# Performance work log

Measured on AMD Instinct MI355X. Metric: run time of the kernel, lower is better.

Reference implementation:

```python
import jax, jax.numpy as jnp
import numpy as np
from jax import lax

BS, NV, CTX = 16, 7, 1536
PLEN, STRIDE = 16, 8
PN = (CTX - PLEN) // STRIDE + 1 + 1  # 192: end replication-pad adds one patch
D, H, DFF, L, TW = 512, 8, 2048, 3, 336
DK = D // H
SCALE = DK ** -0.5  # lsa=False -> fixed scale
NF = D * PN


def setup_inputs() -> dict:
    key = jax.random.key(0)
    ks = iter(jax.random.split(key, 40))

    def p(*shape, s=0.02):
        return jax.random.normal(next(ks), shape, jnp.float32) * s

    z = jax.random.normal(next(ks), (BS, NV, CTX), jnp.float32)
    # simpowerlaw decay mask: -|t|^scale, causal (-inf for k>q), one copy per layer
    t = np.arange(PN)
    times = t[:, None] - t[None, :]
    m = -np.abs(times).astype(np.float32) ** 0.25
    m[times < 0] = -np.inf
    decay_mask = jnp.asarray(np.broadcast_to(m, (L, PN, PN)).copy())
    return dict(
        z=z,
        W_P=p(PLEN, D), b_P=jnp.zeros((D,), jnp.float32),
        W_pos=p(PN, D),
        Wq=p(L, D, D), bq=jnp.zeros((L, D), jnp.float32),
        Wk=p(L, D, D), bk=jnp.zeros((L, D), jnp.float32),
        Wv=p(L, D, D), bv=jnp.zeros((L, D), jnp.float32),
        Wo=p(L, D, D), bo=jnp.zeros((L, D), jnp.float32),
        ln1_g=jnp.ones((L, D), jnp.float32), ln1_b=jnp.zeros((L, D), jnp.float32),
        W1=p(L, D, DFF), b1=jnp.zeros((L, DFF), jnp.float32),
        W2=p(L, DFF, D), b2=jnp.zeros((L, D), jnp.float32),
        ln2_g=jnp.ones((L, D), jnp.float32), ln2_b=jnp.zeros((L, D), jnp.float32),
        W_head=p(NF, TW, s=0.005), b_head=jnp.zeros((TW,), jnp.float32),
        decay_mask=decay_mask,
    )


def _ln(x, g, b):
    mu = x.mean(-1, keepdims=True)
    var = ((x - mu) ** 2).mean(-1, keepdims=True)
    return g * (x - mu) * lax.rsqrt(var + 1e-5) + b


def _forward(z, W_P, b_P, W_pos, Wq, bq, Wk, bk, Wv, bv, Wo, bo,
             ln1_g, ln1_b, W1, b1, W2, b2, ln2_g, ln2_b, W_head, b_head, decay_mask):
    bs, nv, _ = z.shape
    # replication pad end by STRIDE, then unfold into patches
    zp = jnp.concatenate([z, jnp.repeat(z[..., -1:], STRIDE, axis=-1)], axis=-1)
    idx = jnp.arange(PN)[:, None] * STRIDE + jnp.arange(PLEN)[None, :]
    patches = zp[..., idx]                      # [bs,nv,PN,PLEN]
    x = patches @ W_P + b_P                     # [bs,nv,PN,D]
    B = bs * nv
    src = x.reshape(B, PN, D) + W_pos           # channel-independent batch
    prev = jnp.zeros((B, H, PN, PN), src.dtype)  # residual attention carry

    def layer(carry, p):
        s, pr = carry
        wq, bq_, wk, bk_, wv, bv_, wo, bo_, g1, e1, w1, c1, w2, c2, g2, e2, dm = p
        q = (s @ wq + bq_).reshape(B, PN, H, DK).transpose(0, 2, 1, 3)
        k = (s @ wk + bk_).reshape(B, PN, H, DK).transpose(0, 2, 1, 3)
        v = (s @ wv + bv_).reshape(B, PN, H, DK).transpose(0, 2, 1, 3)
        scores = jnp.einsum('bhqd,bhkd->bhqk', q, k) * SCALE + pr + dm
        attn = jax.nn.softmax(scores, axis=-1)
        o = jnp.einsum('bhqk,bhkd->bhqd', attn, v).transpose(0, 2, 1, 3).reshape(B, PN, D)
        o = o @ wo + bo_
        s = _ln(s + o, g1, e1)                  # post-norm
        ff = jax.nn.gelu(s @ w1 + c1, approximate=False) @ w2 + c2
        s = _ln(s + ff, g2, e2)
        return (s, scores), None

    (src, _), _ = lax.scan(
        layer, (src, prev),
        (Wq, bq, Wk, bk, Wv, bv, Wo, bo, ln1_g, ln1_b, W1, b1, W2, b2, ln2_g, ln2_b, decay_mask))

    # Flatten_Head (individual=False): [bs,nv,D,PN] -> [bs,nv,D*PN] -> target_window
    xo = src.reshape(bs, nv, PN, D).transpose(0, 1, 3, 2).reshape(bs, nv, NF)
    return xo @ W_head + b_head                 # [bs,nv,TW]


def reference(z, W_P, b_P, W_pos, Wq, bq, Wk, bk, Wv, bv, Wo, bo,
              ln1_g, ln1_b, W1, b1, W2, b2, ln2_g, ln2_b, W_head, b_head, decay_mask):
    return _forward(z, W_P, b_P, W_pos, Wq, bq, Wk, bk, Wv, bv, Wo, bo,
                    ln1_g, ln1_b, W1, b1, W2, b2, ln2_g, ln2_b, W_head, b_head, decay_mask)
```

## Files before the change

### kernel.cpp

```cpp
#include <hip/hip_runtime.h>
#include <math.h>

#define BSZ 16
#define NV 7
#define CTX 1536
#define PN 192
#define PLEN 16
#define STRIDE 8
#define D 512
#define H 8
#define DK 64
#define DFF 2048
#define LYR 3
#define TW 336
#define NB 112
#define RTOT (NB * PN)
#define NF (D * PN)
#define SCALE 0.125f

typedef __attribute__((ext_vector_type(8))) short s16x8;
typedef __attribute__((ext_vector_type(4))) short s16x4;
typedef __attribute__((ext_vector_type(4))) float f32x4;

__device__ __forceinline__ unsigned short f2b(float f) {
  unsigned u = __builtin_bit_cast(unsigned, f);
  u = u + 0x7fffu + ((u >> 16) & 1u);
  return (unsigned short)(u >> 16);
}
__device__ __forceinline__ float b2f(unsigned short h) {
  unsigned u = ((unsigned)h) << 16;
  return __builtin_bit_cast(float, u);
}
__device__ __forceinline__ unsigned cvtpk(float lo, float hi) {
  unsigned r;
  asm("v_cvt_pk_bf16_f32 %0, %1, %2" : "=v"(r) : "v"(lo), "v"(hi));
  return r;
}
__device__ __forceinline__ float fast_exp2(float x) {
  float r; asm("v_exp_f32 %0, %1" : "=v"(r) : "v"(x)); return r;
}
__device__ __forceinline__ float fast_rcp(float x) {
  float r; asm("v_rcp_f32 %0, %1" : "=v"(r) : "v"(x)); return r;
}

__device__ __forceinline__ void glld(const unsigned short* g, short* l) {
  __builtin_amdgcn_global_load_lds(
      (const __attribute__((address_space(1))) void*)g,
      (__attribute__((address_space(3))) void*)l, 16, 0, 0);
}

__device__ __forceinline__ float gelu(float x) {
  float x2 = x * x;
  float u2 = x * fmaf(0.1029492f, x2, 2.3021186f);
  u2 = fminf(fmaxf(u2, -60.f), 60.f);
  float w = fast_exp2(u2);
  return x * w * fast_rcp(w + 1.0f);
}

__global__ __launch_bounds__(256) void k_patch_embed(
    const float* __restrict__ z, const float* __restrict__ W_P,
    const float* __restrict__ b_P, const float* __restrict__ W_pos,
    unsigned short* __restrict__ s) {
  int r = blockIdx.x;
  int bi = r / PN, p = r % PN;
  __shared__ float pv[PLEN];
  if (threadIdx.x < PLEN) {
    int t = p * STRIDE + threadIdx.x;
    pv[threadIdx.x] = z[(size_t)bi * CTX + (t < CTX ? t : CTX - 1)];
  }
  __syncthreads();
  for (int c = threadIdx.x; c < D; c += 256) {
    float acc = b_P[c] + W_pos[p * D + c];
#pragma unroll
    for (int j = 0; j < PLEN; j++) acc += pv[j] * W_P[j * D + c];
    s[(size_t)r * D + c] = f2b(acc);
  }
}

__global__ __launch_bounds__(256) void k_wtz(
    const float* __restrict__ W, unsigned short* __restrict__ Wt, int K, int N,
    size_t sstride, size_t dstride) {
  __shared__ float tile[32][33];
  const float* Wz = W + (size_t)blockIdx.z * sstride;
  unsigned short* Wtz = Wt + (size_t)blockIdx.z * dstride;
  int n0 = blockIdx.x * 32, k0 = blockIdx.y * 32;
  int tx = threadIdx.x & 31, ty = threadIdx.x >> 5;
#pragma unroll
  for (int i = 0; i < 4; i++)
    tile[ty + 8 * i][tx] =
        (n0 + tx < N) ? Wz[(size_t)(k0 + ty + 8 * i) * N + n0 + tx] : 0.0f;
  __syncthreads();
#pragma unroll
  for (int i = 0; i < 4; i++)
    if (n0 + ty + 8 * i < N)
      Wtz[(size_t)(n0 + ty + 8 * i) * K + k0 + tx] = f2b(tile[tx][ty + 8 * i]);
}

enum { EPI_QKV = 0, EPI_RES = 1, EPI_GELU = 2 };

template <int EPI, int N, int K>
__global__ __launch_bounds__(256) void k_mgemm(
    const unsigned short* __restrict__ Ap, const unsigned short* __restrict__ Wt,
    const float* __restrict__ bias0, const float* __restrict__ bias1,
    const float* __restrict__ bias2, const unsigned short* __restrict__ res,
    unsigned short* __restrict__ out0, unsigned short* __restrict__ out1,
    unsigned short* __restrict__ out2) {
  __shared__ short smem[24576];
  constexpr int NSTEP = K / 32;
  const int nx = N >> 7;
  const int nwg = gridDim.x;
  const int orig = blockIdx.x;
  const int wgid = (orig & 7) * (nwg >> 3) + (orig >> 3);
  const int m0 = (wgid / nx) * 128, n0 = (wgid % nx) * 128;
  const int t = threadIdx.x;
  const int w = t >> 6, l = t & 63;
  const int wr = (w >> 1) * 64, wc = (w & 1) * 64;
  const int lr = l & 15, lq = l >> 4;
  const int rsw = ((lr >> 1) & 3) << 3;
  const int srow = w * 32 + (l >> 2);
  const int scol = 8 * ((l & 3) ^ ((l >> 3) & 3));
  const unsigned short* gA = Ap + (size_t)(m0 + srow) * K + scol;
  const unsigned short* gB = Wt + (size_t)(n0 + srow) * K + scol;
  const int sbo = (w * 32) * 32;
  f32x4 acc[4][4] = {};

  auto STAGE = [&](int b, int kt) {
    short* dA = &smem[b * 8192 + sbo];
    short* dB = &smem[b * 8192 + 4096 + sbo];
    const int k0 = kt * 32;
    glld(gA + k0, dA);
    glld(gA + k0 + (size_t)16 * K, dA + 512);
    glld(gB + k0, dB);
    glld(gB + k0 + (size_t)16 * K, dB + 512);
  };

  STAGE(0, 0);
  STAGE(1, 1);
  int bc = 0, bs = 2;
  for (int step = 0; step < NSTEP; step++) {
    if (step + 2 < NSTEP) STAGE(bs, step + 2);
    if (step + 2 < NSTEP)      asm volatile("s_waitcnt vmcnt(8)" ::: "memory");
    else if (step + 1 < NSTEP) asm volatile("s_waitcnt vmcnt(4)" ::: "memory");
    else                       asm volatile("s_waitcnt vmcnt(0)" ::: "memory");
    __builtin_amdgcn_s_barrier();
    const short* cA = &smem[bc * 8192];
    const short* cB = &smem[bc * 8192 + 4096];
    s16x8 af[4], bf[4];
#pragma unroll
    for (int i = 0; i < 4; i++)
      af[i] = *(const s16x8*)&cA[(wr + i * 16 + lr) * 32 + ((lq * 8) ^ rsw)];
#pragma unroll
    for (int i = 0; i < 4; i++)
      bf[i] = *(const s16x8*)&cB[(wc + i * 16 + lr) * 32 + ((lq * 8) ^ rsw)];
#pragma unroll
    for (int i = 0; i < 4; i++)
#pragma unroll
      for (int j2 = 0; j2 < 4; j2++)
        acc[i][j2] = __builtin_amdgcn_mfma_f32_16x16x32_bf16(bf[j2], af[i], acc[i][j2], 0, 0, 0);
    asm volatile("s_waitcnt lgkmcnt(0)" ::: "memory");
    __builtin_amdgcn_s_barrier();
    bc++; if (bc == 3) bc = 0;
    bs++; if (bs == 3) bs = 0;
  }

  short* ot = smem;
  {
#pragma unroll
    for (int i = 0; i < 4; i++) {
      const int ml = wr + i * 16 + lr;
#pragma unroll
      for (int j2 = 0; j2 < 4; j2++) {
        const int nl = wc + j2 * 16 + lq * 4;
        f32x4 a = acc[i][j2];
        float4 b4 = *(const float4*)&bias0[n0 + nl];
        float v0 = a[0] + b4.x, v1 = a[1] + b4.y;
        float v2 = a[2] + b4.z, v3 = a[3] + b4.w;
        if (EPI == EPI_GELU) {
          v0 = gelu(v0); v1 = gelu(v1); v2 = gelu(v2); v3 = gelu(v3);
        } else {
          s16x4 rr = *(const s16x4*)&res[(size_t)(m0 + ml) * N + n0 + nl];
          v0 += b2f((unsigned short)rr[0]); v1 += b2f((unsigned short)rr[1]);
          v2 += b2f((unsigned short)rr[2]); v3 += b2f((unsigned short)rr[3]);
        }
        unsigned lo = cvtpk(v0, v1), hi = cvtpk(v2, v3);
        unsigned* d = (unsigned*)&ot[ml * 128 + ((nl >> 3) ^ (ml & 15)) * 8 + (nl & 7)];
        d[0] = lo; d[1] = hi;
      }
    }
    __syncthreads();
    const int r0 = t >> 1, cb = (t & 1) * 8;
    const size_t orow = (size_t)(m0 + r0) * N + n0;
#pragma unroll
    for (int q = 0; q < 8; q++) {
      int c = cb + q;
      s16x8 vv = *(const s16x8*)&ot[r0 * 128 + ((c ^ (r0 & 15)) * 8)];
      *(s16x8*)&out0[orow + c * 8] = vv;
    }
  }
}

template <int EPI, int N, int K>
__global__ __launch_bounds__(512, 2) void k_mgemm2(
    const unsigned short* __restrict__ Ap, const unsigned short* __restrict__ Wt,
    const float* __restrict__ bias0, const float* __restrict__ bias1,
    const float* __restrict__ bias2,
    unsigned short* __restrict__ out0, unsigned short* __restrict__ out1,
    unsigned short* __restrict__ out2) {
  __shared__ short smem[65536];
  constexpr int NSTEP = K / 64;
  const int nx = N >> 8;
  const int nwg = gridDim.x;
  const int orig = blockIdx.x;
  const int wgid = (orig & 7) * (nwg >> 3) + (orig >> 3);
  const int m0 = (wgid / nx) * 256, n0 = (wgid % nx) * 256;
  const int t = threadIdx.x;
  const int w = t >> 6, l = t & 63;
  const int wm = w >> 2, wn = w & 3;
  const int lr = l & 15, lq = l >> 4;
  const int srow = (w & 3) * 64 + (l >> 3);
  const int scol = ((l & 7) ^ (l >> 3)) * 8;
  const unsigned short* gsrc =
      (w < 4) ? (Ap + (size_t)(m0 + srow) * K + scol)
              : (Wt + (size_t)(n0 + srow) * K + scol);
  short* sdst = &smem[(w >= 4 ? 16384 : 0) + (w & 3) * 4096];
  f32x4 acc[8][4] = {};

  auto STAGE = [&](int b, int kt) {
    short* d = sdst + b * 32768;
    const unsigned short* g = gsrc + kt * 64;
#pragma unroll
    for (int q = 0; q < 8; q++)
      glld(g + (size_t)q * 8 * K, d + q * 512);
  };

  STAGE(0, 0);
  for (int step = 0; step < NSTEP; step++) {
    const int b = step & 1;
    if (step + 1 < NSTEP) {
      STAGE(b ^ 1, step + 1);
      asm volatile("s_waitcnt vmcnt(8)" ::: "memory");
    } else {
      asm volatile("s_waitcnt vmcnt(0)" ::: "memory");
    }
    __builtin_amdgcn_s_barrier();
    const short* cA = &smem[b * 32768];
    const short* cB = &smem[b * 32768 + 16384];
#pragma unroll
    for (int kk = 0; kk < 2; kk++) {
      s16x8 af[8], bf[4];
#pragma unroll
      for (int i = 0; i < 8; i++)
        af[i] = *(const s16x8*)&cA[(wm * 128 + i * 16 + lr) * 64 +
                                   (((kk * 4 + lq) ^ (lr & 7)) * 8)];
#pragma unroll
      for (int j = 0; j < 4; j++)
        bf[j] = *(const s16x8*)&cB[(wn * 64 + j * 16 + lr) * 64 +
                                   (((kk * 4 + lq) ^ (lr & 7)) * 8)];
      __builtin_amdgcn_s_setprio(1);
#pragma unroll
      for (int i = 0; i < 8; i++)
#pragma unroll
        for (int j = 0; j < 4; j++)
          acc[i][j] = __builtin_amdgcn_mfma_f32_16x16x32_bf16(bf[j], af[i], acc[i][j], 0, 0, 0);
      __builtin_amdgcn_s_setprio(0);
    }
    asm volatile("s_waitcnt lgkmcnt(0)" ::: "memory");
    __builtin_amdgcn_s_barrier();
  }

  short* ot = smem;
  if (EPI == EPI_QKV) {
    const int which = n0 >> 9;
    const int ccb = n0 & 511;
    const float* bias = (which == 0) ? bias0 : (which == 1) ? bias1 : bias2;
    unsigned short* dst = (which == 0) ? out0 : (which == 1) ? out1 : out2;
    if (which < 2) {
#pragma unroll
      for (int i = 0; i < 8; i++) {
        const int ml = wm * 128 + i * 16 + lr;
#pragma unroll
        for (int j = 0; j < 4; j++) {
          const int nl = wn * 64 + j * 16 + lq * 4;
          f32x4 a = acc[i][j];
          float4 b4 = *(const float4*)&bias[ccb + nl];
          unsigned lo = cvtpk(a[0] + b4.x, a[1] + b4.y);
          unsigned hi = cvtpk(a[2] + b4.z, a[3] + b4.w);
          unsigned* d = (unsigned*)&ot[ml * 256 + ((nl >> 3) ^ (ml & 15)) * 8 + (nl & 7)];
          d[0] = lo; d[1] = hi;
        }
      }
      __syncthreads();
      const int r0 = t >> 1, cb = (t & 1) * 16;
      const int m = m0 + r0;
      const int bi2 = m / PN, p = m % PN;
#pragma unroll
      for (int q = 0; q < 16; q++) {
        int c = cb + q;
        int cc = ccb + c * 8;
        int hh = cc >> 6, dk8 = cc & 63;
        s16x8 vv = *(const s16x8*)&ot[r0 * 256 + ((c ^ (r0 & 15)) * 8)];
        *(s16x8*)&dst[(((size_t)bi2 * H + hh) * PN + p) * DK + dk8] = vv;
      }
    } else {
#pragma unroll
      for (int i = 0; i < 8; i++) {
        const int m = m0 + wm * 128 + i * 16 + lr;
        const int bi2 = m / PN, p = m % PN;
#pragma unroll
        for (int j = 0; j < 4; j++) {
          const int nl = wn * 64 + j * 16 + lq * 4;
          f32x4 a = acc[i][j];
#pragma unroll
          for (int r = 0; r < 4; r++) {
            int cc = ccb + nl + r;
            int hh = cc >> 6, dkk = cc & 63;
            dst[(((size_t)bi2 * H + hh) * DK + dkk) * PN + p] = f2b(a[r] + bias[cc]);
          }
        }
      }
    }
  } else {
#pragma unroll
    for (int i = 0; i < 8; i++) {
      const int ml = wm * 128 + i * 16 + lr;
#pragma unroll
      for (int j = 0; j < 4; j++) {
        const int nl = wn * 64 + j * 16 + lq * 4;
        f32x4 a = acc[i][j];
        float4 b4 = *(const float4*)&bias0[n0 + nl];
        float v0 = gelu(a[0] + b4.x), v1 = gelu(a[1] + b4.y);
        float v2 = gelu(a[2] + b4.z), v3 = gelu(a[3] + b4.w);
        unsigned lo = cvtpk(v0, v1), hi = cvtpk(v2, v3);
        unsigned* d = (unsigned*)&ot[ml * 256 + ((nl >> 3) ^ (ml & 15)) * 8 + (nl & 7)];
        d[0] = lo; d[1] = hi;
      }
    }
    __syncthreads();
    const int r0 = t >> 1, cb = (t & 1) * 16;
    const size_t orow = (size_t)(m0 + r0) * N + n0;
#pragma unroll
    for (int q = 0; q < 16; q++) {
      int c = cb + q;
      s16x8 vv = *(const s16x8*)&ot[r0 * 256 + ((c ^ (r0 & 15)) * 8)];
      *(s16x8*)&out0[orow + c * 8] = vv;
    }
  }
}

#define PSTR 196
template <int FIRST, int WRITEC>
__global__ __launch_bounds__(256) void k_attn(
    const unsigned short* __restrict__ qb, const unsigned short* __restrict__ kb,
    const unsigned short* __restrict__ vt, const float* __restrict__ dm,
    unsigned short* __restrict__ carry, unsigned short* __restrict__ ob) {
  __shared__ short Ps[96 * PSTR];
  __shared__ float redmax[2][96];
  __shared__ float redsum[2][96];
  int blk = blockIdx.x;
  int bh = blk >> 1, qh = blk & 1;
  int bi = bh >> 3, h = bh & 7;
  int t = threadIdx.x, w = t >> 6, l = t & 63;
  int wq = w >> 1, wk = w & 1;
  int lr = l & 15, lq = l >> 4, lk = lq * 8;
  const unsigned short* Q = qb + (size_t)bh * PN * DK + (size_t)qh * 96 * DK;
  const unsigned short* K = kb + (size_t)bh * PN * DK;
  f32x4 sv[3][6] = {};
#pragma unroll
  for (int ks = 0; ks < 2; ks++) {
    s16x8 af[3], bf[6];
#pragma unroll
    for (int i = 0; i < 3; i++)
      af[i] = *(const s16x8*)&Q[(size_t)(wq * 48 + i * 16 + lr) * DK + ks * 32 + lk];
#pragma unroll
    for (int j = 0; j < 6; j++)
      bf[j] = *(const s16x8*)&K[(size_t)(wk * 96 + j * 16 + lr) * DK + ks * 32 + lk];
#pragma unroll
    for (int i = 0; i < 3; i++)
#pragma unroll
      for (int j = 0; j < 6; j++)
        sv[i][j] = __builtin_amdgcn_mfma_f32_16x16x32_bf16(af[i], bf[j], sv[i][j], 0, 0, 0);
  }
  size_t cbase = (size_t)blk * 18432 + (size_t)(w * 18) * 256 + (size_t)l * 4;
#pragma unroll
  for (int i = 0; i < 3; i++) {
#pragma unroll
    for (int j = 0; j < 6; j++) {
      s16x4 cv;
      if (!FIRST) cv = *(const s16x4*)&carry[cbase + (i * 6 + j) * 256];
      s16x4 cw;
#pragma unroll
      for (int r = 0; r < 4; r++) {
        int row = qh * 96 + wq * 48 + i * 16 + lq * 4 + r;
        int col = wk * 96 + j * 16 + lr;
        float v = sv[i][j][r] * SCALE + dm[row * PN + col];
        if (!FIRST) v += b2f((unsigned short)cv[r]);
        if (WRITEC) cw[r] = (short)f2b(v);
        sv[i][j][r] = v;
      }
      if (WRITEC) *(s16x4*)&carry[cbase + (i * 6 + j) * 256] = cw;
    }
  }
#pragma unroll
  for (int i = 0; i < 3; i++) {
#pragma unroll
    for (int r = 0; r < 4; r++) {
      float m = sv[i][0][r];
#pragma unroll
      for (int j = 1; j < 6; j++) m = fmaxf(m, sv[i][j][r]);
#pragma unroll
      for (int off = 1; off < 16; off <<= 1) m = fmaxf(m, __shfl_xor(m, off));
      if (lr == 0) redmax[wk][wq * 48 + i * 16 + lq * 4 + r] = m;
    }
  }
  __syncthreads();
#pragma unroll
  for (int i = 0; i < 3; i++) {
#pragma unroll
    for (int r = 0; r < 4; r++) {
      int row = wq * 48 + i * 16 + lq * 4 + r;
      float fm = fmaxf(redmax[0][row], redmax[1][row]);
      float sum = 0.f;
#pragma unroll
      for (int j = 0; j < 6; j++) {
        float e = __expf(sv[i][j][r] - fm);
        sum += e;
        Ps[row * PSTR + wk * 96 + j * 16 + lr] = f2b(e);
      }
#pragma unroll
      for (int off = 1; off < 16; off <<= 1) sum += __shfl_xor(sum, off);
      if (lr == 0) redsum[wk][row] = sum;
    }
  }
  __syncthreads();
  const unsigned short* V = vt + (size_t)bh * DK * PN;
  f32x4 po[3][2] = {};
#pragma unroll
  for (int ks = 0; ks < 6; ks++) {
    s16x8 af[3], bf[2];
#pragma unroll
    for (int i = 0; i < 3; i++)
      af[i] = *(const s16x8*)&Ps[(wq * 48 + i * 16 + lr) * PSTR + ks * 32 + lk];
#pragma unroll
    for (int j = 0; j < 2; j++)
      bf[j] = *(const s16x8*)&V[(size_t)(wk * 32 + j * 16 + lr) * PN + ks * 32 + lk];
#pragma unroll
    for (int i = 0; i < 3; i++)
#pragma unroll
      for (int j = 0; j < 2; j++)
        po[i][j] = __builtin_amdgcn_mfma_f32_16x16x32_bf16(af[i], bf[j], po[i][j], 0, 0, 0);
  }
#pragma unroll
  for (int i = 0; i < 3; i++) {
#pragma unroll
    for (int r = 0; r < 4; r++) {
      int row = wq * 48 + i * 16 + lq * 4 + r;
      float inv = 1.0f / (redsum[0][row] + redsum[1][row]);
#pragma unroll
      for (int j = 0; j < 2; j++) {
        int dk = wk * 32 + j * 16 + lr;
        ob[((size_t)bi * PN + qh * 96 + row) * D + h * 64 + dk] = f2b(po[i][j][r] * inv);
      }
    }
  }
}

__global__ __launch_bounds__(256) void k_ln(
    const unsigned short* __restrict__ in, const float* __restrict__ g,
    const float* __restrict__ b, unsigned short* __restrict__ out) {
  int r = blockIdx.x * 4 + (threadIdx.x >> 6);
  int l = threadIdx.x & 63;
  const unsigned short* x = in + (size_t)r * D + l * 8;
  s16x8 xv = *(const s16x8*)x;
  float v[8], sm = 0.f, sq = 0.f;
#pragma unroll
  for (int j = 0; j < 8; j++) {
    v[j] = b2f((unsigned short)xv[j]);
    sm += v[j];
    sq += v[j] * v[j];
  }
#pragma unroll
  for (int off = 32; off > 0; off >>= 1) {
    sm += __shfl_xor(sm, off);
    sq += __shfl_xor(sq, off);
  }
  float mu = sm * (1.0f / D);
  float rs = rsqrtf(sq * (1.0f / D) - mu * mu + 1e-5f);
  float4 g0 = *(const float4*)&g[l * 8], g1 = *(const float4*)&g[l * 8 + 4];
  float4 b0 = *(const float4*)&b[l * 8], b1 = *(const float4*)&b[l * 8 + 4];
  float gg[8] = {g0.x, g0.y, g0.z, g0.w, g1.x, g1.y, g1.z, g1.w};
  float bb[8] = {b0.x, b0.y, b0.z, b0.w, b1.x, b1.y, b1.z, b1.w};
  s16x8 ov;
#pragma unroll
  for (int j = 0; j < 8; j++) ov[j] = (short)f2b(gg[j] * (v[j] - mu) * rs + bb[j]);
  *(s16x8*)(out + (size_t)r * D + l * 8) = ov;
}

__global__ __launch_bounds__(256) void k_transpose_b(
    const unsigned short* __restrict__ sb, unsigned short* __restrict__ xo) {
  __shared__ unsigned short tile[32][33];
  int d0 = blockIdx.x * 32, p0 = blockIdx.y * 32, bv = blockIdx.z;
  int tx = threadIdx.x & 31, ty = threadIdx.x >> 5;
#pragma unroll
  for (int i = 0; i < 4; i++)
    tile[ty + 8 * i][tx] = sb[((size_t)bv * PN + p0 + ty + 8 * i) * D + d0 + tx];
  __syncthreads();
#pragma unroll
  for (int i = 0; i < 4; i++)
    xo[(size_t)bv * NF + (size_t)(d0 + ty + 8 * i) * PN + p0 + tx] = tile[tx][ty + 8 * i];
}

__global__ __launch_bounds__(448) void k_head_mgemm(
    const unsigned short* __restrict__ A, const unsigned short* __restrict__ B,
    float* __restrict__ pp) {
  __shared__ short As[112 * 40];
  __shared__ short Bs[336 * 40];
  int kc = blockIdx.x;
  int t = threadIdx.x, w = t >> 6, l = t & 63;
  int lr = l & 15, lk = (l >> 4) * 8;
  int ar = t >> 2, ac = (t & 3) * 8;
  f32x4 acc[7][3] = {};
  for (int ks = 0; ks < 24; ks++) {
    int k0 = kc * 768 + ks * 32;
    s16x8 av = *(const s16x8*)&A[(size_t)ar * NF + k0 + ac];
    s16x8 bv0, bv1, bv2;
    {
      int i0 = t, i1 = t + 448, i2 = t + 896;
      bv0 = *(const s16x8*)&B[(size_t)(i0 >> 2) * NF + k0 + (i0 & 3) * 8];
      bv1 = *(const s16x8*)&B[(size_t)(i1 >> 2) * NF + k0 + (i1 & 3) * 8];
      bv2 = *(const s16x8*)&B[(size_t)(i2 >> 2) * NF + k0 + (i2 & 3) * 8];
    }
    __syncthreads();
    *(s16x8*)&As[ar * 40 + ac] = av;
    *(s16x8*)&Bs[(t >> 2) * 40 + (t & 3) * 8] = bv0;
    *(s16x8*)&Bs[((t + 448) >> 2) * 40 + (t & 3) * 8] = bv1;
    *(s16x8*)&Bs[((t + 896) >> 2) * 40 + (t & 3) * 8] = bv2;
    __syncthreads();
    s16x8 bf[3];
#pragma unroll
    for (int j = 0; j < 3; j++)
      bf[j] = *(const s16x8*)&Bs[((w * 3 + j) * 16 + lr) * 40 + lk];
#pragma unroll
    for (int mf = 0; mf < 7; mf++) {
      s16x8 af = *(const s16x8*)&As[(mf * 16 + lr) * 40 + lk];
#pragma unroll
      for (int j = 0; j < 3; j++)
        acc[mf][j] = __builtin_amdgcn_mfma_f32_16x16x32_bf16(af, bf[j], acc[mf][j], 0, 0, 0);
    }
  }
#pragma unroll
  for (int mf = 0; mf < 7; mf++) {
#pragma unroll
    for (int j = 0; j < 3; j++) {
#pragma unroll
      for (int r = 0; r < 4; r++) {
        int row = mf * 16 + (l >> 4) * 4 + r;
        int col = (w * 3 + j) * 16 + lr;
        pp[((size_t)kc * NB + row) * TW + col] = acc[mf][j][r];
      }
    }
  }
}

__global__ __launch_bounds__(256) void k_head_reduce(
    const float* __restrict__ pp, const float* __restrict__ bh,
    float* __restrict__ out) {
  int i = blockIdx.x * 256 + threadIdx.x;
  float s = bh[i % TW];
  for (int kc = 0; kc < 128; kc++) s += pp[(size_t)kc * (NB * TW) + i];
  out[i] = s;
}

extern "C" void kernel_launch(void* const* d_in, const int* in_sizes, int n_in,
                              void* d_out, int out_size, void* d_ws, size_t ws_size,
                              hipStream_t stream) {
  const float* z     = (const float*)d_in[0];
  const float* W_P   = (const float*)d_in[1];
  const float* b_P   = (const float*)d_in[2];
  const float* W_pos = (const float*)d_in[3];
  const float* Wq    = (const float*)d_in[4];
  const float* bq    = (const float*)d_in[5];
  const float* Wk    = (const float*)d_in[6];
  const float* bk    = (const float*)d_in[7];
  const float* Wv    = (const float*)d_in[8];
  const float* bv    = (const float*)d_in[9];
  const float* Wo    = (const float*)d_in[10];
  const float* bo    = (const float*)d_in[11];
  const float* ln1g  = (const float*)d_in[12];
  const float* ln1b  = (const float*)d_in[13];
  const float* W1    = (const float*)d_in[14];
  const float* b1    = (const float*)d_in[15];
  const float* W2    = (const float*)d_in[16];
  const float* b2    = (const float*)d_in[17];
  const float* ln2g  = (const float*)d_in[18];
  const float* ln2b  = (const float*)d_in[19];
  const float* Wh    = (const float*)d_in[20];
  const float* bh    = (const float*)d_in[21];
  const float* dmask = (const float*)d_in[22];
  float* out = (float*)d_out;

  char* ws = (char*)d_ws;
  unsigned short* s  = (unsigned short*)ws;
  unsigned short* sc = (unsigned short*)(ws + 22020096ull);
  unsigned short* qb = (unsigned short*)(ws + 88080384ull);
  unsigned short* kb = (unsigned short*)(ws + 110100480ull);
  unsigned short* vb = (unsigned short*)(ws + 132120576ull);
  unsigned short* ob = (unsigned short*)(ws + 154140672ull);
  unsigned short* tb = (unsigned short*)(ws + 176160768ull);
  unsigned short* hb = qb;
  unsigned short* t2 = tb;
  unsigned short* wt = (unsigned short*)(ws + 198180864ull);
  const size_t WLS = 3145728;
  unsigned short* xo  = (unsigned short*)(ws + 88080384ull);
  unsigned short* Wht = (unsigned short*)(ws + 110100480ull);
  float* pp = (float*)(ws + 22020096ull);

  k_patch_embed<<<RTOT, 256, 0, stream>>>(z, W_P, b_P, W_pos, s);

  k_wtz<<<dim3(16, 16, 3), 256, 0, stream>>>(Wq, wt + 0,       D, D,   262144, WLS);
  k_wtz<<<dim3(16, 16, 3), 256, 0, stream>>>(Wk, wt + 262144,  D, D,   262144, WLS);
  k_wtz<<<dim3(16, 16, 3), 256, 0, stream>>>(Wv, wt + 524288,  D, D,   262144, WLS);
  k_wtz<<<dim3(16, 16, 3), 256, 0, stream>>>(Wo, wt + 786432,  D, D,   262144, WLS);
  k_wtz<<<dim3(64, 16, 3), 256, 0, stream>>>(W1, wt + 1048576, D, DFF, 1048576, WLS);
  k_wtz<<<dim3(16, 64, 3), 256, 0, stream>>>(W2, wt + 2097152, DFF, D, 1048576, WLS);

  for (int l = 0; l < LYR; l++) {
    unsigned short* wtL = wt + (size_t)l * WLS;
    unsigned short* wqkv_t = wtL;
    unsigned short* wo_t   = wtL + 786432;
    unsigned short* w1_t   = wtL + 1048576;
    unsigned short* w2_t   = wtL + 2097152;

    k_mgemm2<EPI_QKV, 1536, 512><<<504, 512, 0, stream>>>(
        s, wqkv_t, bq + l * D, bk + l * D, bv + l * D, qb, kb, vb);
    const float* dm = dmask + (size_t)l * PN * PN;
    if (l == 0)
      k_attn<1, 1><<<NB * H * 2, 256, 0, stream>>>(qb, kb, vb, dm, sc, ob);
    else if (l == LYR - 1)
      k_attn<0, 0><<<NB * H * 2, 256, 0, stream>>>(qb, kb, vb, dm, sc, ob);
    else
      k_attn<0, 1><<<NB * H * 2, 256, 0, stream>>>(qb, kb, vb, dm, sc, ob);
    k_mgemm<EPI_RES, 512, 512><<<672, 256, 0, stream>>>(
        ob, wo_t, bo + l * D, nullptr, nullptr, s, tb, nullptr, nullptr);
    k_ln<<<RTOT / 4, 256, 0, stream>>>(tb, ln1g + l * D, ln1b + l * D, s);
    k_mgemm2<EPI_GELU, 2048, 512><<<672, 512, 0, stream>>>(
        s, w1_t, b1 + l * DFF, nullptr, nullptr, hb, nullptr, nullptr);
    k_mgemm<EPI_RES, 512, 2048><<<672, 256, 0, stream>>>(
        hb, w2_t, b2 + l * D, nullptr, nullptr, s, t2, nullptr, nullptr);
    k_ln<<<RTOT / 4, 256, 0, stream>>>(t2, ln2g + l * D, ln2b + l * D, s);
  }

  k_wtz<<<dim3(11, 3072, 1), 256, 0, stream>>>(Wh, Wht, NF, TW, 0, 0);
  k_transpose_b<<<dim3(16, 6, NB), 256, 0, stream>>>(s, xo);
  k_head_mgemm<<<128, 448, 0, stream>>>(xo, Wht, pp);
  k_head_reduce<<<147, 256, 0, stream>>>(pp, bh, out);
}
```

Measured before the change: 1.106 ms.

## Unify GEMMs into one 256x256 kernel with interleaved LDS-load/MFMA pipeline

Merges the 128x128 and 256x256 GEMM kernels into a single 256x256-tile, 512-thread kernel that handles QKV, residual and GELU epilogues. The main loop is split into four MFMA quadrants, and the next tile's A and B global-to-LDS loads are issued between them so memory traffic overlaps compute. Barriers and s_setprio bracket each quadrant. The output-projection and FFN2 GEMMs (N=512) now use 168 large tiles instead of 672 small ones, which cuts redundant operand loads but leaves fewer workgroups to fill the GPU.

Result: no change. 1.120 ms (+1.3%).

```diff
diff --git a/kernel.cpp b/kernel.cpp
--- a/kernel.cpp
+++ b/kernel.cpp
@@ -99,79 +99,189 @@
 enum { EPI_QKV = 0, EPI_RES = 1, EPI_GELU = 2 };
 
 template <int EPI, int N, int K>
-__global__ __launch_bounds__(256) void k_mgemm(
+__global__ __launch_bounds__(512, 2) void k_mgemm2(
     const unsigned short* __restrict__ Ap, const unsigned short* __restrict__ Wt,
     const float* __restrict__ bias0, const float* __restrict__ bias1,
     const float* __restrict__ bias2, const unsigned short* __restrict__ res,
     unsigned short* __restrict__ out0, unsigned short* __restrict__ out1,
     unsigned short* __restrict__ out2) {
-  __shared__ short smem[24576];
-  constexpr int NSTEP = K / 32;
-  const int nx = N >> 7;
+  __shared__ short smem[65536];
+  constexpr int NT = K / 64;
+  const int nx = N >> 8;
   const int nwg = gridDim.x;
   const int orig = blockIdx.x;
   const int wgid = (orig & 7) * (nwg >> 3) + (orig >> 3);
-  const int m0 = (wgid / nx) * 128, n0 = (wgid % nx) * 128;
+  const int m0 = (wgid / nx) * 256, n0 = (wgid % nx) * 256;
   const int t = threadIdx.x;
   const int w = t >> 6, l = t & 63;
-  const int wr = (w >> 1) * 64, wc = (w & 1) * 64;
+  const int wm = w >> 2, wn = w & 3;
   const int lr = l & 15, lq = l >> 4;
-  const int rsw = ((lr >> 1) & 3) << 3;
-  const int srow = w * 32 + (l >> 2);
-  const int scol = 8 * ((l & 3) ^ ((l >> 3) & 3));
-  const unsigned short* gA = Ap + (size_t)(m0 + srow) * K + scol;
-  const unsigned short* gB = Wt + (size_t)(n0 + srow) * K + scol;
-  const int sbo = (w * 32) * 32;
-  f32x4 acc[4][4] = {};
-
-  auto STAGE = [&](int b, int kt) {
-    short* dA = &smem[b * 8192 + sbo];
-    short* dB = &smem[b * 8192 + 4096 + sbo];
-    const int k0 = kt * 32;
-    glld(gA + k0, dA);
-    glld(gA + k0 + (size_t)16 * K, dA + 512);
-    glld(gB + k0, dB);
-    glld(gB + k0 + (size_t)16 * K, dB + 512);
+  const int sr8 = w * 8 + (l >> 3);
+  const int sc8 = ((l & 7) ^ ((l >> 3) & 7)) * 8;
+  const unsigned short* gAs = Ap + (size_t)(m0 + sr8) * K + sc8;
+  const unsigned short* gBs = Wt + (size_t)(n0 + sr8) * K + sc8;
+  f32x4 acc[8][4] = {};
+
+  auto STA = [&](int bb, int kt, int h) {
+    short* d = &smem[bb * 32768 + (h * 128 + w * 8) * 64];
+    const unsigned short* g = gAs + (size_t)(h * 128) * K + kt * 64;
+    glld(g, d);
+    glld(g + (size_t)64 * K, d + 4096);
   };
-
-  STAGE(0, 0);
-  STAGE(1, 1);
-  int bc = 0, bs = 2;
-  for (int step = 0; step < NSTEP; step++) {
-    if (step + 2 < NSTEP) STAGE(bs, step + 2);
-    if (step + 2 < NSTEP)      asm volatile("s_waitcnt vmcnt(8)" ::: "memory");
-    else if (step + 1 < NSTEP) asm volatile("s_waitcnt vmcnt(4)" ::: "memory");
-    else                       asm volatile("s_waitcnt vmcnt(0)" ::: "memory");
+  auto STB = [&](int bb, int kt, int h) {
+    short* d = &smem[bb * 32768 + 16384 + (h * 128 + w * 8) * 64];
+    const unsigned short* g = gBs + (size_t)(h * 128) * K + kt * 64;
+    glld(g, d);
+    glld(g + (size_t)64 * K, d + 4096);
+  };
+
+  STA(0, 0, 0); STA(0, 0, 1); STB(0, 0, 0); STB(0, 0, 1);
+  asm volatile("s_waitcnt vmcnt(0)" ::: "memory");
+  __builtin_amdgcn_s_barrier();
+
+  for (int kt = 0; kt < NT; kt++) {
+    const int bb = kt & 1;
+    const short* cA = &smem[bb * 32768];
+    const short* cB = &smem[bb * 32768 + 16384];
+    s16x8 af0[4][2], af1[4][2], bf0[2][2], bf1[2][2];
+#pragma unroll
+    for (int i = 0; i < 4; i++)
+#pragma unroll
+      for (int kk = 0; kk < 2; kk++)
+        af0[i][kk] = *(const s16x8*)&cA[(wm * 128 + i * 16 + lr) * 64 +
+                                        (((kk * 4 + lq) ^ (lr & 7)) * 8)];
+#pragma unroll
+    for (int j = 0; j < 2; j++)
+#pragma unroll
+      for (int kk = 0; kk < 2; kk++)
+        bf0[j][kk] = *(const s16x8*)&cB[(wn * 64 + j * 16 + lr) * 64 +
+                                        (((kk * 4 + lq) ^ (lr & 7)) * 8)];
+    if (kt + 1 < NT) { STA(bb ^ 1, kt + 1, 0); STA(bb ^ 1, kt + 1, 1); }
     __builtin_amdgcn_s_barrier();
-    const short* cA = &smem[bc * 8192];
-    const short* cB = &smem[bc * 8192 + 4096];
-    s16x8 af[4], bf[4];
+    asm volatile("s_waitcnt lgkmcnt(0)" ::: "memory");
+    __builtin_amdgcn_s_setprio(1);
+#pragma unroll
+    for (int kk = 0; kk < 2; kk++)
+#pragma unroll
+      for (int i = 0; i < 4; i++)
+#pragma unroll
+        for (int j = 0; j < 2; j++)
+          acc[i][j] = __builtin_amdgcn_mfma_f32_16x16x32_bf16(
+              bf0[j][kk], af0[i][kk], acc[i][j], 0, 0, 0);
+    __builtin_amdgcn_s_setprio(0);
+    __builtin_amdgcn_s_barrier();
+#pragma unroll
+    for (int j = 0; j < 2; j++)
+#pragma unroll
+      for (int kk = 0; kk < 2; kk++)
+        bf1[j][kk] = *(const s16x8*)&cB[(wn * 64 + (2 + j) * 16 + lr) * 64 +
+                                        (((kk * 4 + lq) ^ (lr & 7)) * 8)];
+    if (kt + 1 < NT) { STB(bb ^ 1, kt + 1, 0); STB(bb ^ 1, kt + 1, 1); }
+    __builtin_amdgcn_s_barrier();
+    asm volatile("s_waitcnt lgkmcnt(0)" ::: "memory");
+    __builtin_amdgcn_s_setprio(1);
+#pragma unroll
+    for (int kk = 0; kk < 2; kk++)
+#pragma unroll
+      for (int i = 0; i < 4; i++)
+#pragma unroll
+        for (int j = 0; j < 2; j++)
+          acc[i][2 + j] = __builtin_amdgcn_mfma_f32_16x16x32_bf16(
+              bf1[j][kk], af0[i][kk], acc[i][2 + j], 0, 0, 0);
+    __builtin_amdgcn_s_setprio(0);
+    __builtin_amdgcn_s_barrier();
 #pragma unroll
     for (int i = 0; i < 4; i++)
-      af[i] = *(const s16x8*)&cA[(wr + i * 16 + lr) * 32 + ((lq * 8) ^ rsw)];
-#pragma unroll
-    for (int i = 0; i < 4; i++)
-      bf[i] = *(const s16x8*)&cB[(wc + i * 16 + lr) * 32 + ((lq * 8) ^ rsw)];
-#pragma unroll
-    for (int i = 0; i < 4; i++)
-#pragma unroll
-      for (int j2 = 0; j2 < 4; j2++)
-        acc[i][j2] = __builtin_amdgcn_mfma_f32_16x16x32_bf16(bf[j2], af[i], acc[i][j2], 0, 0, 0);
+#pragma unroll
+      for (int kk = 0; kk < 2; kk++)
+        af1[i][kk] = *(const s16x8*)&cA[(wm * 128 + 64 + i * 16 + lr) * 64 +
+                                        (((kk * 4 + lq) ^ (lr & 7)) * 8)];
+    __builtin_amdgcn_s_barrier();
     asm volatile("s_waitcnt lgkmcnt(0)" ::: "memory");
+    __builtin_amdgcn_s_setprio(1);
+#pragma unroll
+    for (int kk = 0; kk < 2; kk++)
+#pragma unroll
+      for (int i = 0; i < 4; i++)
+#pragma unroll
+        for (int j = 0; j < 2; j++)
+          acc[4 + i][j] = __builtin_amdgcn_mfma_f32_16x16x32_bf16(
+              bf0[j][kk], af1[i][kk], acc[4 + i][j], 0, 0, 0);
+    __builtin_amdgcn_s_setprio(0);
     __builtin_amdgcn_s_barrier();
-    bc++; if (bc == 3) bc = 0;
-    bs++; if (bs == 3) bs = 0;
+    __builtin_amdgcn_s_setprio(1);
+#pragma unroll
+    for (int kk = 0; kk < 2; kk++)
+#pragma unroll
+      for (int i = 0; i < 4; i++)
+#pragma unroll
+        for (int j = 0; j < 2; j++)
+          acc[4 + i][2 + j] = __builtin_amdgcn_mfma_f32_16x16x32_bf16(
+              bf1[j][kk], af1[i][kk], acc[4 + i][2 + j], 0, 0, 0);
+    __builtin_amdgcn_s_setprio(0);
+    asm volatile("s_waitcnt vmcnt(0)" ::: "memory");
+    __builtin_amdgcn_s_barrier();
   }
 
   short* ot = smem;
-  {
-#pragma unroll
-    for (int i = 0; i < 4; i++) {
-      const int ml = wr + i * 16 + lr;
-#pragma unroll
-      for (int j2 = 0; j2 < 4; j2++) {
-        const int nl = wc + j2 * 16 + lq * 4;
-        f32x4 a = acc[i][j2];
+  if (EPI == EPI_QKV) {
+    const int which = n0 >> 9;
+    const int ccb = n0 & 511;
+    const float* bias = (which == 0) ? bias0 : (which == 1) ? bias1 : bias2;
+    unsigned short* dst = (which == 0) ? out0 : (which == 1) ? out1 : out2;
+    if (which < 2) {
+#pragma unroll
+      for (int i = 0; i < 8; i++) {
+        const int ml = wm * 128 + i * 16 + lr;
+#pragma unroll
+        for (int j = 0; j < 4; j++) {
+          const int nl = wn * 64 + j * 16 + lq * 4;
+          f32x4 a = acc[i][j];
+          float4 b4 = *(const float4*)&bias[ccb + nl];
+          unsigned lo = cvtpk(a[0] + b4.x, a[1] + b4.y);
+          unsigned hi = cvtpk(a[2] + b4.z, a[3] + b4.w);
+          unsigned* d = (unsigned*)&ot[ml * 256 + ((nl >> 3) ^ (ml & 15)) * 8 + (nl & 7)];
+          d[0] = lo; d[1] = hi;
+        }
+      }
+      __syncthreads();
+      const int r0 = t >> 1, cb = (t & 1) * 16;
+      const int m = m0 + r0;
+      const int bi2 = m / PN, p = m % PN;
+#pragma unroll
+      for (int q = 0; q < 16; q++) {
+        int c = cb + q;
+        int cc = ccb + c * 8;
+        int hh = cc >> 6, dk8 = cc & 63;
+        s16x8 vv = *(const s16x8*)&ot[r0 * 256 + ((c ^ (r0 & 15)) * 8)];
+        *(s16x8*)&dst[(((size_t)bi2 * H + hh) * PN + p) * DK + dk8] = vv;
+      }
+    } else {
+#pragma unroll
+      for (int i = 0; i < 8; i++) {
+        const int m = m0 + wm * 128 + i * 16 + lr;
+        const int bi2 = m / PN, p = m % PN;
+#pragma unroll
+        for (int j = 0; j < 4; j++) {
+          const int nl = wn * 64 + j * 16 + lq * 4;
+          f32x4 a = acc[i][j];
+#pragma unroll
+          for (int r = 0; r < 4; r++) {
+            int cc = ccb + nl + r;
+            int hh = cc >> 6, dkk = cc & 63;
+            dst[(((size_t)bi2 * H + hh) * DK + dkk) * PN + p] = f2b(a[r] + bias[cc]);
+          }
+        }
+      }
+    }
+  } else {
+#pragma unroll
+    for (int i = 0; i < 8; i++) {
+      const int ml = wm * 128 + i * 16 + lr;
+#pragma unroll
+      for (int j = 0; j < 4; j++) {
+        const int nl = wn * 64 + j * 16 + lq * 4;
+        f32x4 a = acc[i][j];
         float4 b4 = *(const float4*)&bias0[n0 + nl];
         float v0 = a[0] + b4.x, v1 = a[1] + b4.y;
         float v2 = a[2] + b4.z, v3 = a[3] + b4.w;
@@ -182,154 +292,6 @@
           v0 += b2f((unsigned short)rr[0]); v1 += b2f((unsigned short)rr[1]);
           v2 += b2f((unsigned short)rr[2]); v3 += b2f((unsigned short)rr[3]);
         }
-        unsigned lo = cvtpk(v0, v1), hi = cvtpk(v2, v3);
-        unsigned* d = (unsigned*)&ot[ml * 128 + ((nl >> 3) ^ (ml & 15)) * 8 + (nl & 7)];
-        d[0] = lo; d[1] = hi;
-      }
-    }
-    __syncthreads();
-    const int r0 = t >> 1, cb = (t & 1) * 8;
-    const size_t orow = (size_t)(m0 + r0) * N + n0;
-#pragma unroll
-    for (int q = 0; q < 8; q++) {
-      int c = cb + q;
-      s16x8 vv = *(const s16x8*)&ot[r0 * 128 + ((c ^ (r0 & 15)) * 8)];
-      *(s16x8*)&out0[orow + c * 8] = vv;
-    }
-  }
-}
-
-template <int EPI, int N, int K>
-__global__ __launch_bounds__(512, 2) void k_mgemm2(
-    const unsigned short* __restrict__ Ap, const unsigned short* __restrict__ Wt,
-    const float* __restrict__ bias0, const float* __restrict__ bias1,
-    const float* __restrict__ bias2,
-    unsigned short* __restrict__ out0, unsigned short* __restrict__ out1,
-    unsigned short* __restrict__ out2) {
-  __shared__ short smem[65536];
-  constexpr int NSTEP = K / 64;
-  const int nx = N >> 8;
-  const int nwg = gridDim.x;
-  const int orig = blockIdx.x;
-  const int wgid = (orig & 7) * (nwg >> 3) + (orig >> 3);
-  const int m0 = (wgid / nx) * 256, n0 = (wgid % nx) * 256;
-  const int t = threadIdx.x;
-  const int w = t >> 6, l = t & 63;
-  const int wm = w >> 2, wn = w & 3;
-  const int lr = l & 15, lq = l >> 4;
-  const int srow = (w & 3) * 64 + (l >> 3);
-  const int scol = ((l & 7) ^ (l >> 3)) * 8;
-  const unsigned short* gsrc =
-      (w < 4) ? (Ap + (size_t)(m0 + srow) * K + scol)
-              : (Wt + (size_t)(n0 + srow) * K + scol);
-  short* sdst = &smem[(w >= 4 ? 16384 : 0) + (w & 3) * 4096];
-  f32x4 acc[8][4] = {};
-
-  auto STAGE = [&](int b, int kt) {
-    short* d = sdst + b * 32768;
-    const unsigned short* g = gsrc + kt * 64;
-#pragma unroll
-    for (int q = 0; q < 8; q++)
-      glld(g + (size_t)q * 8 * K, d + q * 512);
-  };
-
-  STAGE(0, 0);
-  for (int step = 0; step < NSTEP; step++) {
-    const int b = step & 1;
-    if (step + 1 < NSTEP) {
-      STAGE(b ^ 1, step + 1);
-      asm volatile("s_waitcnt vmcnt(8)" ::: "memory");
-    } else {
-      asm volatile("s_waitcnt vmcnt(0)" ::: "memory");
-    }
-    __builtin_amdgcn_s_barrier();
-    const short* cA = &smem[b * 32768];
-    const short* cB = &smem[b * 32768 + 16384];
-#pragma unroll
-    for (int kk = 0; kk < 2; kk++) {
-      s16x8 af[8], bf[4];
-#pragma unroll
-      for (int i = 0; i < 8; i++)
-        af[i] = *(const s16x8*)&cA[(wm * 128 + i * 16 + lr) * 64 +
-                                   (((kk * 4 + lq) ^ (lr & 7)) * 8)];
-#pragma unroll
-      for (int j = 0; j < 4; j++)
-        bf[j] = *(const s16x8*)&cB[(wn * 64 + j * 16 + lr) * 64 +
-                                   (((kk * 4 + lq) ^ (lr & 7)) * 8)];
-      __builtin_amdgcn_s_setprio(1);
-#pragma unroll
-      for (int i = 0; i < 8; i++)
-#pragma unroll
-        for (int j = 0; j < 4; j++)
-          acc[i][j] = __builtin_amdgcn_mfma_f32_16x16x32_bf16(bf[j], af[i], acc[i][j], 0, 0, 0);
-      __builtin_amdgcn_s_setprio(0);
-    }
-    asm volatile("s_waitcnt lgkmcnt(0)" ::: "memory");
-    __builtin_amdgcn_s_barrier();
-  }
-
-  short* ot = smem;
-  if (EPI == EPI_QKV) {
-    const int which = n0 >> 9;
-    const int ccb = n0 & 511;
-    const float* bias = (which == 0) ? bias0 : (which == 1) ? bias1 : bias2;
-    unsigned short* dst = (which == 0) ? out0 : (which == 1) ? out1 : out2;
-    if (which < 2) {
-#pragma unroll
-      for (int i = 0; i < 8; i++) {
-        const int ml = wm * 128 + i * 16 + lr;
-#pragma unroll
-        for (int j = 0; j < 4; j++) {
-          const int nl = wn * 64 + j * 16 + lq * 4;
-          f32x4 a = acc[i][j];
-          float4 b4 = *(const float4*)&bias[ccb + nl];
-          unsigned lo = cvtpk(a[0] + b4.x, a[1] + b4.y);
-          unsigned hi = cvtpk(a[2] + b4.z, a[3] + b4.w);
-          unsigned* d = (unsigned*)&ot[ml * 256 + ((nl >> 3) ^ (ml & 15)) * 8 + (nl & 7)];
-          d[0] = lo; d[1] = hi;
-        }
-      }
-      __syncthreads();
-      const int r0 = t >> 1, cb = (t & 1) * 16;
-      const int m = m0 + r0;
-      const int bi2 = m / PN, p = m % PN;
-#pragma unroll
-      for (int q = 0; q < 16; q++) {
-        int c = cb + q;
-        int cc = ccb + c * 8;
-        int hh = cc >> 6, dk8 = cc & 63;
-        s16x8 vv = *(const s16x8*)&ot[r0 * 256 + ((c ^ (r0 & 15)) * 8)];
-        *(s16x8*)&dst[(((size_t)bi2 * H + hh) * PN + p) * DK + dk8] = vv;
-      }
-    } else {
-#pragma unroll
-      for (int i = 0; i < 8; i++) {
-        const int m = m0 + wm * 128 + i * 16 + lr;
-        const int bi2 = m / PN, p = m % PN;
-#pragma unroll
-        for (int j = 0; j < 4; j++) {
-          const int nl = wn * 64 + j * 16 + lq * 4;
-          f32x4 a = acc[i][j];
-#pragma unroll
-          for (int r = 0; r < 4; r++) {
-            int cc = ccb + nl + r;
-            int hh = cc >> 6, dkk = cc & 63;
-            dst[(((size_t)bi2 * H + hh) * DK + dkk) * PN + p] = f2b(a[r] + bias[cc]);
-          }
-        }
-      }
-    }
-  } else {
-#pragma unroll
-    for (int i = 0; i < 8; i++) {
-      const int ml = wm * 128 + i * 16 + lr;
-#pragma unroll
-      for (int j = 0; j < 4; j++) {
-        const int nl = wn * 64 + j * 16 + lq * 4;
-        f32x4 a = acc[i][j];
-        float4 b4 = *(const float4*)&bias0[n0 + nl];
-        float v0 = gelu(a[0] + b4.x), v1 = gelu(a[1] + b4.y);
-        float v2 = gelu(a[2] + b4.z), v3 = gelu(a[3] + b4.w);
         unsigned lo = cvtpk(v0, v1), hi = cvtpk(v2, v3);
         unsigned* d = (unsigned*)&ot[ml * 256 + ((nl >> 3) ^ (ml & 15)) * 8 + (nl & 7)];
         d[0] = lo; d[1] = hi;
@@ -631,7 +593,7 @@
     unsigned short* w2_t   = wtL + 2097152;
 
     k_mgemm2<EPI_QKV, 1536, 512><<<504, 512, 0, stream>>>(
-        s, wqkv_t, bq + l * D, bk + l * D, bv + l * D, qb, kb, vb);
+        s, wqkv_t, bq + l * D, bk + l * D, bv + l * D, nullptr, qb, kb, vb);
     const float* dm = dmask + (size_t)l * PN * PN;
     if (l == 0)
       k_attn<1, 1><<<NB * H * 2, 256, 0, stream>>>(qb, kb, vb, dm, sc, ob);
@@ -639,12 +601,12 @@
       k_attn<0, 0><<<NB * H * 2, 256, 0, stream>>>(qb, kb, vb, dm, sc, ob);
     else
       k_attn<0, 1><<<NB * H * 2, 256, 0, stream>>>(qb, kb, vb, dm, sc, ob);
-    k_mgemm<EPI_RES, 512, 512><<<672, 256, 0, stream>>>(
+    k_mgemm2<EPI_RES, 512, 512><<<168, 512, 0, stream>>>(
         ob, wo_t, bo + l * D, nullptr, nullptr, s, tb, nullptr, nullptr);
     k_ln<<<RTOT / 4, 256, 0, stream>>>(tb, ln1g + l * D, ln1b + l * D, s);
     k_mgemm2<EPI_GELU, 2048, 512><<<672, 512, 0, stream>>>(
-        s, w1_t, b1 + l * DFF, nullptr, nullptr, hb, nullptr, nullptr);
-    k_mgemm<EPI_RES, 512, 2048><<<672, 256, 0, stream>>>(
+        s, w1_t, b1 + l * DFF, nullptr, nullptr, nullptr, hb, nullptr, nullptr);
+    k_mgemm2<EPI_RES, 512, 2048><<<168, 512, 0, stream>>>(
         hb, w2_t, b2 + l * D, nullptr, nullptr, s, t2, nullptr, nullptr);
     k_ln<<<RTOT / 4, 256, 0, stream>>>(t2, ln2g + l * D, ln2b + l * D, s);
   }
```
